# Performance work log

Measured on AMD Instinct MI355X. Metric: run time of the kernel, lower is better.

## Reference

```python
import jax, jax.numpy as jnp
import numpy as np

WSCALE = 0.05  # keep ReLU MLP activations in a sane range


def setup_inputs() -> dict:
    key = jax.random.key(0)
    ks = jax.random.split(key, 9)
    B, D, H = 2048, 64, 512
    return {
        "x": jax.random.normal(ks[0], (B, D), dtype=jnp.float32),
        "W1": jax.random.normal(ks[1], (H, D), dtype=jnp.float32) * WSCALE,
        "b1": jax.random.normal(ks[2], (H,), dtype=jnp.float32) * WSCALE,
        "W2": jax.random.normal(ks[3], (H, H), dtype=jnp.float32) * WSCALE,
        "b2": jax.random.normal(ks[4], (H,), dtype=jnp.float32) * WSCALE,
        "W3": jax.random.normal(ks[5], (H, H), dtype=jnp.float32) * WSCALE,
        "b3": jax.random.normal(ks[6], (H,), dtype=jnp.float32) * WSCALE,
        "W4": jax.random.normal(ks[7], (D, H), dtype=jnp.float32) * WSCALE,
        "b4": jax.random.normal(ks[8], (D,), dtype=jnp.float32) * WSCALE,
    }


def reference(x, W1, b1, W2, b2, W3, b3, W4, b4):
    # Score network: ReLU MLP (weights stored PyTorch-style [out, in]).
    a1 = x @ W1.T + b1          # [B, H]
    h1 = jax.nn.relu(a1)
    a2 = h1 @ W2.T + b2
    h2 = jax.nn.relu(a2)
    a3 = h2 @ W3.T + b3
    h3 = jax.nn.relu(a3)
    s = h3 @ W4.T + b4          # [B, D] score

    # Divergence = trace of Jacobian ds/dx per sample.
    # Per-sample J = W4 @ diag(m3) @ W3 @ diag(m2) @ W2 @ diag(m1) @ W1,
    # with m_k = 1[a_k > 0] (ReLU derivative; 0 at 0 like torch autograd).
    m1 = (a1 > 0).astype(x.dtype)
    m2 = (a2 > 0).astype(x.dtype)
    m3 = (a3 > 0).astype(x.dtype)
    T = m1[:, :, None] * W1[None, :, :]                 # [B, H, D]
    T = m2[:, :, None] * jnp.einsum('ij,bjd->bid', W2, T)  # [B, H, D]
    T = m3[:, :, None] * jnp.einsum('ij,bjd->bid', W3, T)  # [B, H, D]
    div = jnp.einsum('dj,bjd->b', W4, T)                # trace of J, [B]

    # Hyvarinen score: 0.5 * ||s||^2 + div
    val = 0.5 * jnp.sum(s * s, axis=1) + div
    return val
```

## Files before the change

### kernel.cpp

```cpp
#include <hip/hip_runtime.h>
#include <stdint.h>


typedef __attribute__((ext_vector_type(8))) short short8;
typedef __attribute__((ext_vector_type(4))) float f32x4;

union U16x8 {
  uint4 u;
  short8 s;
};

__device__ __forceinline__ uint16_t f2bf(float f) {
  uint32_t u = __float_as_uint(f);
  uint32_t lsb = (u >> 16) & 1u;
  u += 0x7FFFu + lsb;
  return (uint16_t)(u >> 16);
}

__global__ __launch_bounds__(256) void convert_kernel(
    const float* __restrict__ W1, const float* __restrict__ W2,
    const float* __restrict__ W3, const float* __restrict__ W4,
    uint16_t* __restrict__ A2swz, uint16_t* __restrict__ A3swz,
    uint16_t* __restrict__ B1swz, uint16_t* __restrict__ B4swz,
    float* __restrict__ W2Tf, float* __restrict__ W3Tf,
    float* __restrict__ W1Tf, float* __restrict__ W4Tf) {
  const int i = blockIdx.x * 256 + threadIdx.x;
  if (i < 262144) {
    const int e = i;
    const int f = e >> 3, j = e & 7;
    const int lane = f & 63, fk = f >> 6;
    const int kc = fk & 15, r16 = fk >> 4;
    const int l15 = lane & 15, quad = lane >> 4;
    const int row = r16 * 16 + l15, col = kc * 32 + quad * 8 + j;
    A2swz[e] = f2bf(W2[row * 512 + col]);
  } else if (i < 524288) {
    const int e = i - 262144;
    const int f = e >> 3, j = e & 7;
    const int lane = f & 63, fk = f >> 6;
    const int kc = fk & 15, r16 = fk >> 4;
    const int l15 = lane & 15, quad = lane >> 4;
    const int row = r16 * 16 + l15, col = kc * 32 + quad * 8 + j;
    A3swz[e] = f2bf(W3[col * 512 + row]);
  } else if (i < 557056) {
    const int e = i - 524288;
    const int f = e >> 3, j = e & 7;
    const int lane = f & 63, fk = f >> 6;
    const int kc = fk >> 2, jt = fk & 3;
    const int l15 = lane & 15, quad = lane >> 4;
    const int d = jt * 16 + l15, col = kc * 32 + quad * 8 + j;
    B1swz[e] = f2bf(W1[col * 64 + d]);
  } else if (i < 589824) {
    const int e = i - 557056;
    const int f = e >> 3, j = e & 7;
    const int lane = f & 63, fk = f >> 6;
    const int kc = fk >> 2, jt = fk & 3;
    const int l15 = lane & 15, quad = lane >> 4;
    const int d = jt * 16 + l15, col = kc * 32 + quad * 8 + j;
    B4swz[e] = f2bf(W4[d * 512 + col]);
  } else if (i < 851968) {
    const int e = i - 589824;
    const int k = e >> 9, jj = e & 511;
    W2Tf[e] = W2[jj * 512 + k];
  } else if (i < 1114112) {
    const int e = i - 851968;
    const int k = e >> 9, jj = e & 511;
    W3Tf[e] = W3[jj * 512 + k];
  } else if (i < 1146880) {
    const int e = i - 1114112;
    const int k = e >> 9, jj = e & 511;
    W1Tf[e] = W1[jj * 64 + k];
  } else if (i < 1179648) {
    const int e = i - 1146880;
    const int k = e >> 6, d = e & 63;
    W4Tf[e] = W4[d * 512 + k];
  }
}

__device__ __forceinline__ void fwd_hidden(
    const float* __restrict__ WT, const float* __restrict__ bias,
    const float4* __restrict__ src, float4* __restrict__ dst,
    uint32_t* __restrict__ mw, uint32_t* __restrict__ mglob,
    int sh, int jq, int t, int K) {
  const int j4 = jq * 4;
  float a[4][4];
  {
    const float4 bb = *(const float4*)(bias + j4);
#pragma unroll
    for (int si = 0; si < 4; ++si) {
      a[0][si] = bb.x; a[1][si] = bb.y; a[2][si] = bb.z; a[3][si] = bb.w;
    }
  }
#pragma unroll 4
  for (int k = 0; k < K; ++k) {
    const float4 w = *(const float4*)(WT + (size_t)k * 512 + j4);
    const float4 h = src[k];
    a[0][0] = fmaf(w.x, h.x, a[0][0]); a[0][1] = fmaf(w.x, h.y, a[0][1]);
    a[0][2] = fmaf(w.x, h.z, a[0][2]); a[0][3] = fmaf(w.x, h.w, a[0][3]);
    a[1][0] = fmaf(w.y, h.x, a[1][0]); a[1][1] = fmaf(w.y, h.y, a[1][1]);
    a[1][2] = fmaf(w.y, h.z, a[1][2]); a[1][3] = fmaf(w.y, h.w, a[1][3]);
    a[2][0] = fmaf(w.z, h.x, a[2][0]); a[2][1] = fmaf(w.z, h.y, a[2][1]);
    a[2][2] = fmaf(w.z, h.z, a[2][2]); a[2][3] = fmaf(w.z, h.w, a[2][3]);
    a[3][0] = fmaf(w.w, h.x, a[3][0]); a[3][1] = fmaf(w.w, h.y, a[3][1]);
    a[3][2] = fmaf(w.w, h.z, a[3][2]); a[3][3] = fmaf(w.w, h.w, a[3][3]);
  }
  const int word = jq >> 3, shift = 4 * (jq & 7);
#pragma unroll
  for (int si = 0; si < 4; ++si) {
    uint32_t nib = (a[0][si] > 0.f ? 1u : 0u) | (a[1][si] > 0.f ? 2u : 0u) |
                   (a[2][si] > 0.f ? 4u : 0u) | (a[3][si] > 0.f ? 8u : 0u);
    if (nib) atomicOr(&mw[(sh * 4 + si) * 16 + word], nib << shift);
  }
#pragma unroll
  for (int u = 0; u < 4; ++u) {
    float4 r;
    r.x = a[u][0] > 0.f ? a[u][0] : 0.f;
    r.y = a[u][1] > 0.f ? a[u][1] : 0.f;
    r.z = a[u][2] > 0.f ? a[u][2] : 0.f;
    r.w = a[u][3] > 0.f ? a[u][3] : 0.f;
    dst[j4 + u] = r;
  }
  __syncthreads();
  if (t < 128) {
    mglob[(size_t)(t >> 4) * 16 + (t & 15)] = mw[t];
    mw[t] = 0;
  }
  __syncthreads();
}

__global__ __launch_bounds__(256) void forward_kernel(
    const float* __restrict__ x,
    const float* __restrict__ W1Tf, const float* __restrict__ b1,
    const float* __restrict__ W2Tf, const float* __restrict__ b2,
    const float* __restrict__ W3Tf, const float* __restrict__ b3,
    const float* __restrict__ W4Tf, const float* __restrict__ b4,
    uint32_t* __restrict__ m1p, uint32_t* __restrict__ m2p,
    uint32_t* __restrict__ m3p, float* __restrict__ out) {
  __shared__ float4 xs[2][64];
  __shared__ float4 hp[2][2][512];
  __shared__ uint32_t mw[128];
  const int t = threadIdx.x;
  const int b0 = blockIdx.x * 8;
  const int sh = t >> 7;
  const int jq = t & 127;

  {
#pragma unroll
    for (int r = 0; r < 2; ++r) {
      const int i = t * 2 + r;
      const int k = i >> 3, s = i & 7;
      ((float*)&xs[s >> 2][k])[s & 3] = x[(size_t)(b0 + s) * 64 + k];
    }
    if (t < 128) mw[t] = 0;
  }
  __syncthreads();

  fwd_hidden(W1Tf, b1, xs[sh], hp[0][sh], mw, m1p + (size_t)b0 * 16, sh, jq, t, 64);
  fwd_hidden(W2Tf, b2, hp[0][sh], hp[1][sh], mw, m2p + (size_t)b0 * 16, sh, jq, t, 512);
  fwd_hidden(W3Tf, b3, hp[1][sh], hp[0][sh], mw, m3p + (size_t)b0 * 16, sh, jq, t, 512);

  {
    const int wv = t >> 6, lane = t & 63;
    const int d = lane;
    const int s0 = wv * 2, s1 = s0 + 1;
    const float* h0 = (const float*)&hp[0][s0 >> 2][0] + (s0 & 3);
    const float* h1 = (const float*)&hp[0][s1 >> 2][0] + (s1 & 3);
    float acc0 = b4[d], acc1 = b4[d];
#pragma unroll 8
    for (int k = 0; k < 512; ++k) {
      const float w = W4Tf[k * 64 + d];
      acc0 = fmaf(w, h0[k * 4], acc0);
      acc1 = fmaf(w, h1[k * 4], acc1);
    }
    float sq0 = acc0 * acc0, sq1 = acc1 * acc1;
#pragma unroll
    for (int off = 32; off; off >>= 1) {
      sq0 += __shfl_down(sq0, off, 64);
      sq1 += __shfl_down(sq1, off, 64);
    }
    if (lane == 0) {
      out[b0 + s0] = 0.5f * sq0;
      out[b0 + s1] = 0.5f * sq1;
    }
  }
}

__device__ __forceinline__ void expand_mask(uint32_t byte8, uint32_t mk[4]) {
#pragma unroll
  for (int i = 0; i < 4; ++i) {
    mk[i] = (((byte8 >> (2 * i)) & 1u) ? 0x0000FFFFu : 0u) |
            (((byte8 >> (2 * i + 1)) & 1u) ? 0xFFFF0000u : 0u);
  }
}

__global__ __launch_bounds__(256, 2) void div_kernel(
    const uint4* __restrict__ A2swz, const uint4* __restrict__ A3swz,
    const uint4* __restrict__ B1swz, const uint4* __restrict__ B4swz,
    const uint32_t* __restrict__ m1p, const uint32_t* __restrict__ m2p,
    const uint32_t* __restrict__ m3p, float* __restrict__ out) {
  const int t = threadIdx.x;
  const int lane = t & 63, wv = t >> 6;
  const int sLoc = wv & 1, rh = wv >> 1;
  const int l15 = lane & 15, quad = lane >> 4;
  const int g = blockIdx.x;
  const int rowB0 = blockIdx.y * 128;
  const int b = g * 2 + sLoc;
  const int r16b = (rowB0 >> 4) + rh * 4;

  f32x4 accC[4][4], accG[4][4];
#pragma unroll
  for (int it = 0; it < 4; ++it)
#pragma unroll
    for (int jt = 0; jt < 4; ++jt) {
      accC[it][jt] = (f32x4){0.f, 0.f, 0.f, 0.f};
      accG[it][jt] = (f32x4){0.f, 0.f, 0.f, 0.f};
    }

  const uint32_t* m1w = m1p + (size_t)b * 16;
  const uint32_t* m3w = m3p + (size_t)b * 16;

#pragma unroll 1
  for (int kc = 0; kc < 16; ++kc) {
    uint4 a2[4], u1[4], a3[4], u4[4];
#pragma unroll
    for (int it = 0; it < 4; ++it)
      a2[it] = A2swz[(size_t)((r16b + it) * 16 + kc) * 64 + lane];
#pragma unroll
    for (int jt = 0; jt < 4; ++jt)
      u1[jt] = B1swz[(size_t)(kc * 4 + jt) * 64 + lane];
#pragma unroll
    for (int it = 0; it < 4; ++it)
      a3[it] = A3swz[(size_t)((r16b + it) * 16 + kc) * 64 + lane];
#pragma unroll
    for (int jt = 0; jt < 4; ++jt)
      u4[jt] = B4swz[(size_t)(kc * 4 + jt) * 64 + lane];

    const uint32_t m1d = __builtin_amdgcn_readfirstlane(m1w[kc]);
    const uint32_t m3d = __builtin_amdgcn_readfirstlane(m3w[kc]);
    uint32_t mk1[4], mk3[4];
    expand_mask((m1d >> (quad * 8)) & 0xFFu, mk1);
    expand_mask((m3d >> (quad * 8)) & 0xFFu, mk3);

    short8 bC[4];
#pragma unroll
    for (int jt = 0; jt < 4; ++jt) {
      U16x8 u;
      u.u = u1[jt];
      u.u.x &= mk1[0]; u.u.y &= mk1[1]; u.u.z &= mk1[2]; u.u.w &= mk1[3];
      bC[jt] = u.s;
    }
#pragma unroll
    for (int it = 0; it < 4; ++it) {
      U16x8 ua;
      ua.u = a2[it];
      const short8 af = ua.s;
#pragma unroll
      for (int jt = 0; jt < 4; ++jt)
        accC[it][jt] = __builtin_amdgcn_mfma_f32_16x16x32_bf16(af, bC[jt], accC[it][jt], 0, 0, 0);
    }
    short8 bG[4];
#pragma unroll
    for (int jt = 0; jt < 4; ++jt) {
      U16x8 u;
      u.u = u4[jt];
      u.u.x &= mk3[0]; u.u.y &= mk3[1]; u.u.z &= mk3[2]; u.u.w &= mk3[3];
      bG[jt] = u.s;
    }
#pragma unroll
    for (int it = 0; it < 4; ++it) {
      U16x8 ua;
      ua.u = a3[it];
      const short8 af = ua.s;
#pragma unroll
      for (int jt = 0; jt < 4; ++jt)
        accG[it][jt] = __builtin_amdgcn_mfma_f32_16x16x32_bf16(af, bG[jt], accG[it][jt], 0, 0, 0);
    }
  }

  const uint32_t* m2w = m2p + (size_t)b * 16;
  float dsum = 0.f;
#pragma unroll
  for (int it = 0; it < 4; ++it) {
    const int rloc = rh * 64 + it * 16 + quad * 4;
    const uint32_t md = m2w[(rowB0 + rloc) >> 5];
    const uint32_t bits = (md >> (rloc & 31)) & 0xFu;
    const float w0 = (bits & 1u) ? 1.f : 0.f;
    const float w1 = (bits & 2u) ? 1.f : 0.f;
    const float w2 = (bits & 4u) ? 1.f : 0.f;
    const float w3 = (bits & 8u) ? 1.f : 0.f;
#pragma unroll
    for (int jt = 0; jt < 4; ++jt) {
      dsum = fmaf(w0, accC[it][jt][0] * accG[it][jt][0], dsum);
      dsum = fmaf(w1, accC[it][jt][1] * accG[it][jt][1], dsum);
      dsum = fmaf(w2, accC[it][jt][2] * accG[it][jt][2], dsum);
      dsum = fmaf(w3, accC[it][jt][3] * accG[it][jt][3], dsum);
    }
  }
#pragma unroll
  for (int off = 32; off; off >>= 1) dsum += __shfl_down(dsum, off, 64);
  if (lane == 0) atomicAdd(out + b, dsum);
}

extern "C" void kernel_launch(void* const* d_in, const int* in_sizes, int n_in,
                              void* d_out, int out_size, void* d_ws, size_t ws_size,
                              hipStream_t stream) {
  const float* x  = (const float*)d_in[0];
  const float* W1 = (const float*)d_in[1];
  const float* b1 = (const float*)d_in[2];
  const float* W2 = (const float*)d_in[3];
  const float* b2 = (const float*)d_in[4];
  const float* W3 = (const float*)d_in[5];
  const float* b3 = (const float*)d_in[6];
  const float* W4 = (const float*)d_in[7];
  const float* b4 = (const float*)d_in[8];
  float* out = (float*)d_out;

  char* ws = (char*)d_ws;
  uint16_t* A2swz = (uint16_t*)(ws + 0);
  uint16_t* A3swz = (uint16_t*)(ws + 524288);
  uint16_t* B1swz = (uint16_t*)(ws + 1048576);
  uint16_t* B4swz = (uint16_t*)(ws + 1114112);
  float*    W2Tf  = (float*)(ws + 1179648);
  float*    W3Tf  = (float*)(ws + 2228224);
  float*    W1Tf  = (float*)(ws + 3276800);
  float*    W4Tf  = (float*)(ws + 3407872);
  uint32_t* m1p   = (uint32_t*)(ws + 3538944);
  uint32_t* m2p   = (uint32_t*)(ws + 3670016);
  uint32_t* m3p   = (uint32_t*)(ws + 3801088);
  if (ws_size < 3932160) return;

  convert_kernel<<<4608, 256, 0, stream>>>(W1, W2, W3, W4,
                                           A2swz, A3swz, B1swz, B4swz,
                                           W2Tf, W3Tf, W1Tf, W4Tf);
  forward_kernel<<<256, 256, 0, stream>>>(x, W1Tf, b1, W2Tf, b2, W3Tf, b3,
                                          W4Tf, b4, m1p, m2p, m3p, out);
  div_kernel<<<dim3(1024, 4), 256, 0, stream>>>((const uint4*)A2swz,
                                                (const uint4*)A3swz,
                                                (const uint4*)B1swz,
                                                (const uint4*)B4swz,
                                                m1p, m2p, m3p, out);
}
```

Measured before the change: 326.1 us.

## Double threads per block in forward and divergence kernels, halving per-thread sample work

```diff
diff --git a/kernel.cpp b/kernel.cpp
--- a/kernel.cpp
+++ b/kernel.cpp
@@ -76,58 +76,7 @@
   }
 }
 
-__device__ __forceinline__ void fwd_hidden(
-    const float* __restrict__ WT, const float* __restrict__ bias,
-    const float4* __restrict__ src, float4* __restrict__ dst,
-    uint32_t* __restrict__ mw, uint32_t* __restrict__ mglob,
-    int sh, int jq, int t, int K) {
-  const int j4 = jq * 4;
-  float a[4][4];
-  {
-    const float4 bb = *(const float4*)(bias + j4);
-#pragma unroll
-    for (int si = 0; si < 4; ++si) {
-      a[0][si] = bb.x; a[1][si] = bb.y; a[2][si] = bb.z; a[3][si] = bb.w;
-    }
-  }
-#pragma unroll 4
-  for (int k = 0; k < K; ++k) {
-    const float4 w = *(const float4*)(WT + (size_t)k * 512 + j4);
-    const float4 h = src[k];
-    a[0][0] = fmaf(w.x, h.x, a[0][0]); a[0][1] = fmaf(w.x, h.y, a[0][1]);
-    a[0][2] = fmaf(w.x, h.z, a[0][2]); a[0][3] = fmaf(w.x, h.w, a[0][3]);
-    a[1][0] = fmaf(w.y, h.x, a[1][0]); a[1][1] = fmaf(w.y, h.y, a[1][1]);
-    a[1][2] = fmaf(w.y, h.z, a[1][2]); a[1][3] = fmaf(w.y, h.w, a[1][3]);
-    a[2][0] = fmaf(w.z, h.x, a[2][0]); a[2][1] = fmaf(w.z, h.y, a[2][1]);
-    a[2][2] = fmaf(w.z, h.z, a[2][2]); a[2][3] = fmaf(w.z, h.w, a[2][3]);
-    a[3][0] = fmaf(w.w, h.x, a[3][0]); a[3][1] = fmaf(w.w, h.y, a[3][1]);
-    a[3][2] = fmaf(w.w, h.z, a[3][2]); a[3][3] = fmaf(w.w, h.w, a[3][3]);
-  }
-  const int word = jq >> 3, shift = 4 * (jq & 7);
-#pragma unroll
-  for (int si = 0; si < 4; ++si) {
-    uint32_t nib = (a[0][si] > 0.f ? 1u : 0u) | (a[1][si] > 0.f ? 2u : 0u) |
-                   (a[2][si] > 0.f ? 4u : 0u) | (a[3][si] > 0.f ? 8u : 0u);
-    if (nib) atomicOr(&mw[(sh * 4 + si) * 16 + word], nib << shift);
-  }
-#pragma unroll
-  for (int u = 0; u < 4; ++u) {
-    float4 r;
-    r.x = a[u][0] > 0.f ? a[u][0] : 0.f;
-    r.y = a[u][1] > 0.f ? a[u][1] : 0.f;
-    r.z = a[u][2] > 0.f ? a[u][2] : 0.f;
-    r.w = a[u][3] > 0.f ? a[u][3] : 0.f;
-    dst[j4 + u] = r;
-  }
-  __syncthreads();
-  if (t < 128) {
-    mglob[(size_t)(t >> 4) * 16 + (t & 15)] = mw[t];
-    mw[t] = 0;
-  }
-  __syncthreads();
-}
-
-__global__ __launch_bounds__(256) void forward_kernel(
+__global__ __launch_bounds__(512) void forward_kernel(
     const float* __restrict__ x,
     const float* __restrict__ W1Tf, const float* __restrict__ b1,
     const float* __restrict__ W2Tf, const float* __restrict__ b2,
@@ -135,52 +84,76 @@
     const float* __restrict__ W4Tf, const float* __restrict__ b4,
     uint32_t* __restrict__ m1p, uint32_t* __restrict__ m2p,
     uint32_t* __restrict__ m3p, float* __restrict__ out) {
-  __shared__ float4 xs[2][64];
-  __shared__ float4 hp[2][2][512];
+  __shared__ float2 xs2[4][64];
+  __shared__ float2 hp[2][4][512];
   __shared__ uint32_t mw[128];
   const int t = threadIdx.x;
   const int b0 = blockIdx.x * 8;
-  const int sh = t >> 7;
-  const int jq = t & 127;
+  const int g = t >> 7;
+  const int q = t & 127;
+  const int j4 = q * 4;
+  const int word = q >> 3, shift = (q & 7) * 4;
 
   {
-#pragma unroll
-    for (int r = 0; r < 2; ++r) {
-      const int i = t * 2 + r;
-      const int k = i >> 3, s = i & 7;
-      ((float*)&xs[s >> 2][k])[s & 3] = x[(size_t)(b0 + s) * 64 + k];
-    }
+    const int s = t >> 6, k = t & 63;
+    ((float*)&xs2[s >> 1][k])[s & 1] = x[(size_t)(b0 + s) * 64 + k];
     if (t < 128) mw[t] = 0;
   }
   __syncthreads();
 
-  fwd_hidden(W1Tf, b1, xs[sh], hp[0][sh], mw, m1p + (size_t)b0 * 16, sh, jq, t, 64);
-  fwd_hidden(W2Tf, b2, hp[0][sh], hp[1][sh], mw, m2p + (size_t)b0 * 16, sh, jq, t, 512);
-  fwd_hidden(W3Tf, b3, hp[1][sh], hp[0][sh], mw, m3p + (size_t)b0 * 16, sh, jq, t, 512);
+  float a[4][2];
+
+#define FWD_LAYER(WT, BIAS, SRC, DSTBUF, MGLOB, KDIM)                          \
+  {                                                                            \
+    const float4 bb = *(const float4*)((BIAS) + j4);                           \
+    a[0][0] = bb.x; a[0][1] = bb.x; a[1][0] = bb.y; a[1][1] = bb.y;            \
+    a[2][0] = bb.z; a[2][1] = bb.z; a[3][0] = bb.w; a[3][1] = bb.w;            \
+    _Pragma("unroll 4") for (int k = 0; k < (KDIM); ++k) {                     \
+      const float4 w = *(const float4*)((WT) + (size_t)k * 512 + j4);          \
+      const float2 h = (SRC)[k];                                               \
+      a[0][0] = fmaf(w.x, h.x, a[0][0]); a[0][1] = fmaf(w.x, h.y, a[0][1]);    \
+      a[1][0] = fmaf(w.y, h.x, a[1][0]); a[1][1] = fmaf(w.y, h.y, a[1][1]);    \
+      a[2][0] = fmaf(w.z, h.x, a[2][0]); a[2][1] = fmaf(w.z, h.y, a[2][1]);    \
+      a[3][0] = fmaf(w.w, h.x, a[3][0]); a[3][1] = fmaf(w.w, h.y, a[3][1]);    \
+    }                                                                          \
+    uint32_t nib0 = (a[0][0] > 0.f ? 1u : 0u) | (a[1][0] > 0.f ? 2u : 0u) |    \
+                    (a[2][0] > 0.f ? 4u : 0u) | (a[3][0] > 0.f ? 8u : 0u);     \
+    uint32_t nib1 = (a[0][1] > 0.f ? 1u : 0u) | (a[1][1] > 0.f ? 2u : 0u) |    \
+                    (a[2][1] > 0.f ? 4u : 0u) | (a[3][1] > 0.f ? 8u : 0u);     \
+    if (nib0) atomicOr(&mw[(2 * g) * 16 + word], nib0 << shift);               \
+    if (nib1) atomicOr(&mw[(2 * g + 1) * 16 + word], nib1 << shift);           \
+    _Pragma("unroll") for (int u = 0; u < 4; ++u) {                            \
+      hp[DSTBUF][g][j4 + u] =                                                  \
+          make_float2(a[u][0] > 0.f ? a[u][0] : 0.f,                           \
+                      a[u][1] > 0.f ? a[u][1] : 0.f);                          \
+    }                                                                          \
+    __syncthreads();                                                           \
+    if (t < 128) {                                                             \
+      (MGLOB)[(size_t)(b0 + (t >> 4)) * 16 + (t & 15)] = mw[t];                \
+      mw[t] = 0;                                                               \
+    }                                                                          \
+    __syncthreads();                                                           \
+  }
+
+  FWD_LAYER(W1Tf, b1, xs2[g], 0, m1p, 64)
+  FWD_LAYER(W2Tf, b2, hp[0][g], 1, m2p, 512)
+  FWD_LAYER(W3Tf, b3, hp[1][g], 0, m3p, 512)
+#undef FWD_LAYER
 
   {
     const int wv = t >> 6, lane = t & 63;
     const int d = lane;
-    const int s0 = wv * 2, s1 = s0 + 1;
-    const float* h0 = (const float*)&hp[0][s0 >> 2][0] + (s0 & 3);
-    const float* h1 = (const float*)&hp[0][s1 >> 2][0] + (s1 & 3);
-    float acc0 = b4[d], acc1 = b4[d];
-#pragma unroll 8
+    const int gg = wv >> 1, c = wv & 1;
+    float acc = b4[d];
+#pragma unroll 4
     for (int k = 0; k < 512; ++k) {
-      const float w = W4Tf[k * 64 + d];
-      acc0 = fmaf(w, h0[k * 4], acc0);
-      acc1 = fmaf(w, h1[k * 4], acc1);
-    }
-    float sq0 = acc0 * acc0, sq1 = acc1 * acc1;
-#pragma unroll
-    for (int off = 32; off; off >>= 1) {
-      sq0 += __shfl_down(sq0, off, 64);
-      sq1 += __shfl_down(sq1, off, 64);
-    }
-    if (lane == 0) {
-      out[b0 + s0] = 0.5f * sq0;
-      out[b0 + s1] = 0.5f * sq1;
-    }
+      const float h = ((const float*)&hp[0][gg][k])[c];
+      acc = fmaf(W4Tf[k * 64 + d], h, acc);
+    }
+    float sq = acc * acc;
+#pragma unroll
+    for (int off = 32; off; off >>= 1) sq += __shfl_down(sq, off, 64);
+    if (d == 0) out[b0 + wv] = 0.5f * sq;
   }
 }
 
@@ -192,18 +165,18 @@
   }
 }
 
-__global__ __launch_bounds__(256, 2) void div_kernel(
+__global__ __launch_bounds__(512, 2) void div_kernel(
     const uint4* __restrict__ A2swz, const uint4* __restrict__ A3swz,
     const uint4* __restrict__ B1swz, const uint4* __restrict__ B4swz,
     const uint32_t* __restrict__ m1p, const uint32_t* __restrict__ m2p,
     const uint32_t* __restrict__ m3p, float* __restrict__ out) {
   const int t = threadIdx.x;
   const int lane = t & 63, wv = t >> 6;
-  const int sLoc = wv & 1, rh = wv >> 1;
+  const int sLoc = wv & 3, rh = wv >> 2;
   const int l15 = lane & 15, quad = lane >> 4;
   const int g = blockIdx.x;
   const int rowB0 = blockIdx.y * 128;
-  const int b = g * 2 + sLoc;
+  const int b = g * 4 + sLoc;
   const int r16b = (rowB0 >> 4) + rh * 4;
 
   f32x4 accC[4][4], accG[4][4];
@@ -331,11 +304,11 @@
   convert_kernel<<<4608, 256, 0, stream>>>(W1, W2, W3, W4,
                                            A2swz, A3swz, B1swz, B4swz,
                                            W2Tf, W3Tf, W1Tf, W4Tf);
-  forward_kernel<<<256, 256, 0, stream>>>(x, W1Tf, b1, W2Tf, b2, W3Tf, b3,
+  forward_kernel<<<256, 512, 0, stream>>>(x, W1Tf, b1, W2Tf, b2, W3Tf, b3,
                                           W4Tf, b4, m1p, m2p, m3p, out);
-  div_kernel<<<dim3(1024, 4), 256, 0, stream>>>((const uint4*)A2swz,
-                                                (const uint4*)A3swz,
-                                                (const uint4*)B1swz,
-                                                (const uint4*)B4swz,
-                                                m1p, m2p, m3p, out);
-}
+  div_kernel<<<dim3(512, 4), 512, 0, stream>>>((const uint4*)A2swz,
+                                               (const uint4*)A3swz,
+                                               (const uint4*)B1swz,
+                                               (const uint4*)B4swz,
+                                               m1p, m2p, m3p, out);
+}
```

After: 344.4 us. 5.6% more time.
